# Kernel tuning notes

Measured on AMD Instinct MI355X. Metric: run time of the kernel, lower is better.

## Reference

```python
import jax, jax.numpy as jnp
import numpy as np

T, B, D = 256, 64, 512


def setup_inputs() -> dict:
    key = jax.random.key(0)
    ks = jax.random.split(key, 9)
    s = 1.0 / np.sqrt(D)  # torch Linear default init scale (uniform), use scaled normal
    return {
        "x": jax.random.normal(ks[0], (T, B, D), dtype=jnp.float32),
        "y": jax.random.normal(ks[1], (T, B, D), dtype=jnp.float32),
        "Wr": jax.random.normal(ks[2], (D, D), dtype=jnp.float32) * s,
        "Ur": jax.random.normal(ks[3], (D, D), dtype=jnp.float32) * s,
        "Wz": jax.random.normal(ks[4], (D, D), dtype=jnp.float32) * s,
        "Uz": jax.random.normal(ks[5], (D, D), dtype=jnp.float32) * s,
        "Wg": jax.random.normal(ks[6], (D, D), dtype=jnp.float32) * s,
        "Ug": jax.random.normal(ks[7], (D, D), dtype=jnp.float32) * s,
        "bg": jnp.full((D,), 2.0, dtype=jnp.float32),
    }


def reference(x, y, Wr, Ur, Wz, Uz, Wg, Ug, bg):
    # GTrXL gating unit. torch Linear(y) == y @ W.T
    r = jax.nn.sigmoid(jnp.einsum("tbd,ed->tbe", y, Wr) + jnp.einsum("tbd,ed->tbe", x, Ur))
    z = jax.nn.sigmoid(jnp.einsum("tbd,ed->tbe", y, Wz) + jnp.einsum("tbd,ed->tbe", x, Uz) - bg)
    h = jnp.tanh(jnp.einsum("tbd,ed->tbe", y, Wg) + jnp.einsum("tbd,ed->tbe", r * x, Ug))
    g = (1.0 - z) * x + z * h  # (T, B, D)
    return g
```

## Files before the change

kernel.cpp:

```cpp
#include <hip/hip_runtime.h>
#include <stdint.h>

typedef unsigned short u16;
typedef __attribute__((ext_vector_type(8))) __bf16 bf16x8;
typedef __attribute__((ext_vector_type(4))) float f32x4;

#define Dn 512
#define Mn 16384


__device__ __forceinline__ u16 f2bf(float f) {
  unsigned u = __float_as_uint(f);
  u += 0x7fffu + ((u >> 16) & 1u);
  return (u16)(u >> 16);
}

__device__ __forceinline__ float bf2f(u16 b) {
  return __uint_as_float(((unsigned)b) << 16);
}

__device__ __forceinline__ void async16(const u16* g, u16* l) {
  __builtin_amdgcn_global_load_lds(
      (const __attribute__((address_space(1))) unsigned int*)g,
      (__attribute__((address_space(3))) unsigned int*)l, 16, 0, 0);
}

__device__ __forceinline__ float sigmoidf_(float v) {
  return 1.f / (1.f + __expf(-v));
}

__global__ void cast_all(const float* __restrict__ y, const float* __restrict__ x,
                         const float* w0, const float* w1, const float* w2,
                         const float* w3, const float* w4, const float* w5,
                         u16* __restrict__ yb, u16* __restrict__ xb,
                         u16* __restrict__ bRZ, u16* __restrict__ bG) {
  int b = blockIdx.x;
  const int t = (int)threadIdx.x;
  if (b < 16384) {
    const float* src;
    u16* dst;
    if (b < 8192) { src = y; dst = yb; }
    else          { src = x; dst = xb; b -= 8192; }
    const int i4 = b * 256 + t;
    float4 v = ((const float4*)src)[i4];
    ushort4 o;
    o.x = f2bf(v.x); o.y = f2bf(v.y); o.z = f2bf(v.z); o.w = f2bf(v.w);
    ((ushort4*)dst)[i4] = o;
    return;
  }
  b -= 16384;
  const int wi = b >> 8;
  const int bb = b & 255;
  const float* src = wi == 0 ? w0 : wi == 1 ? w1 : wi == 2 ? w2
                   : wi == 3 ? w3 : wi == 4 ? w4 : w5;
  const int i4 = bb * 256 + t;
  const int e  = i4 >> 7;
  const int c4 = i4 & 127;
  float4 v = ((const float4*)src)[i4];
  ushort4 o;
  o.x = f2bf(v.x); o.y = f2bf(v.y); o.z = f2bf(v.z); o.w = f2bf(v.w);
  ushort4* base = (wi >= 4) ? (ushort4*)bG : (ushort4*)bRZ;
  const int row = e + ((wi == 2 || wi == 3) ? 512 : 0);
  const int off = row * 256 + c4 + ((wi & 1) ? 128 : 0);
  base[off] = o;
}

__global__ __launch_bounds__(512, 2) void gemm_rz2(
    const u16* __restrict__ yb, const u16* __restrict__ xb,
    const u16* __restrict__ bRZ, const float* __restrict__ bg,
    u16* __restrict__ rxb, u16* __restrict__ zb) {
  __shared__ u16 smem[65536];

  const int tid = threadIdx.x;
  const int lane = tid & 63;
  const int wave = tid >> 6;
  const int waveM = wave >> 2;
  const int waveN = wave & 3;
  const int mb = blockIdx.x & 63, nb = blockIdx.x >> 6;
  const int rowStart = mb * 256, colStart = nb * 256;
  const int lm = lane & 15, quad = lane >> 4;
  const int aoff = (quad ^ ((lm >> 1) & 3)) * 8;

  const int srow = tid >> 2;
  const int lc = ((tid & 3) ^ ((srow >> 1) & 3)) * 8;
  const int woff = wave * 1024;

  f32x4 acc[8][4] = {};

  auto STAGE = [&](int t) {
    const u16* abase = (t < 16) ? yb : xb;
    const int k0 = (t & 15) * 32;
    char* s = (char*)(smem + ((t & 3) << 14));
    async16(abase + (size_t)(rowStart + srow) * 512 + k0 + lc, (u16*)(s + woff));
    async16(abase + (size_t)(rowStart + 128 + srow) * 512 + k0 + lc, (u16*)(s + 8192 + woff));
    async16(bRZ + (size_t)(colStart + srow) * 1024 + t * 32 + lc, (u16*)(s + 16384 + woff));
    async16(bRZ + (size_t)(colStart + 128 + srow) * 1024 + t * 32 + lc, (u16*)(s + 24576 + woff));
  };

  STAGE(0); STAGE(1); STAGE(2); STAGE(3);
  __builtin_amdgcn_sched_barrier(0);

  for (int t = 0; t < 32; ++t) {
    if (t < 29)       asm volatile("s_waitcnt vmcnt(12)" ::: "memory");
    else if (t == 29) asm volatile("s_waitcnt vmcnt(8)" ::: "memory");
    else if (t == 30) asm volatile("s_waitcnt vmcnt(4)" ::: "memory");
    else              asm volatile("s_waitcnt vmcnt(0)" ::: "memory");
    __builtin_amdgcn_sched_barrier(0);
    __builtin_amdgcn_s_barrier();

    const u16* sA = smem + ((t & 3) << 14);
    const u16* sB = sA + 8192;
    bf16x8 aa[8], bw[4];
#pragma unroll
    for (int i = 0; i < 8; ++i)
      aa[i] = *(const bf16x8*)(sA + (waveM * 128 + i * 16 + lm) * 32 + aoff);
#pragma unroll
    for (int j = 0; j < 4; ++j)
      bw[j] = *(const bf16x8*)(sB + (waveN * 64 + j * 16 + lm) * 32 + aoff);
    asm volatile("s_waitcnt lgkmcnt(0)" ::: "memory");
    __builtin_amdgcn_sched_barrier(0);
    __builtin_amdgcn_s_barrier();

    if (t < 28) STAGE(t + 4);
    __builtin_amdgcn_sched_barrier(0);

    __builtin_amdgcn_s_setprio(1);
#pragma unroll
    for (int i = 0; i < 8; ++i)
#pragma unroll
      for (int j = 0; j < 4; ++j)
        acc[i][j] = __builtin_amdgcn_mfma_f32_16x16x32_bf16(aa[i], bw[j], acc[i][j], 0, 0, 0);
    __builtin_amdgcn_s_setprio(0);
  }

  if (colStart < 512) {
#pragma unroll
    for (int j = 0; j < 4; ++j) {
      const int e = colStart + waveN * 64 + j * 16 + lm;
#pragma unroll
      for (int i = 0; i < 8; ++i) {
        const int m0 = rowStart + waveM * 128 + i * 16 + quad * 4;
#pragma unroll
        for (int rg = 0; rg < 4; ++rg) {
          const size_t idx = (size_t)(m0 + rg) * 512 + e;
          const float r = sigmoidf_(acc[i][j][rg]);
          rxb[idx] = f2bf(r * bf2f(xb[idx]));
        }
      }
    }
  } else {
#pragma unroll
    for (int j = 0; j < 4; ++j) {
      const int e = colStart - 512 + waveN * 64 + j * 16 + lm;
      const float bgv = bg[e];
#pragma unroll
      for (int i = 0; i < 8; ++i) {
        const int m0 = rowStart + waveM * 128 + i * 16 + quad * 4;
#pragma unroll
        for (int rg = 0; rg < 4; ++rg) {
          const size_t idx = (size_t)(m0 + rg) * 512 + e;
          zb[idx] = f2bf(sigmoidf_(acc[i][j][rg] - bgv));
        }
      }
    }
  }
}

__global__ __launch_bounds__(256, 4) void gemm_gu1(
    const u16* __restrict__ yb, const u16* __restrict__ rxb,
    const u16* __restrict__ bG,
    const u16* __restrict__ zb, const u16* __restrict__ xb,
    float* __restrict__ out) {
  __shared__ u16 smem[16384];
  u16* sA = smem;
  u16* sB = smem + 8192;

  const int tid = threadIdx.x;
  const int lane = tid & 63;
  const int wave = tid >> 6;
  const int waveM = wave >> 1, waveN = wave & 1;
  const int mb = blockIdx.x & 127, nb = blockIdx.x >> 7;
  const int rowStart = mb * 128, colStart = nb * 128;
  const int wbyte = (tid & 192) * 16;
  const int lm = lane & 15, quad = lane >> 4;

  const int srow = tid >> 3;
  const int scol = (((tid & 7) ^ ((tid >> 3) & 7)) * 8);
  const int lswz = lm & 7;

  f32x4 acc[4][4] = {};

  for (int kq = 0; kq < 16; ++kq) {
    const int half = kq >> 3;
    const int k0 = (kq & 7) * 64;
    const u16* abase = half ? rxb : yb;
#pragma unroll
    for (int s = 0; s < 4; ++s) {
      async16(abase + (size_t)(rowStart + s * 32 + srow) * 512 + k0 + scol,
              (u16*)((char*)sA + s * 4096 + wbyte));
      async16(bG + (size_t)(colStart + s * 32 + srow) * 1024 + kq * 64 + scol,
              (u16*)((char*)sB + s * 4096 + wbyte));
    }
    __syncthreads();

#pragma unroll
    for (int kk = 0; kk < 2; ++kk) {
      bf16x8 aa[4], bw[4];
#pragma unroll
      for (int i = 0; i < 4; ++i)
        aa[i] = *(const bf16x8*)(sA + (waveM * 64 + i * 16 + lm) * 64 +
                                 ((kk * 4 + quad) ^ lswz) * 8);
#pragma unroll
      for (int j = 0; j < 4; ++j)
        bw[j] = *(const bf16x8*)(sB + (waveN * 64 + j * 16 + lm) * 64 +
                                 ((kk * 4 + quad) ^ lswz) * 8);
#pragma unroll
      for (int i = 0; i < 4; ++i)
#pragma unroll
        for (int j = 0; j < 4; ++j)
          acc[i][j] = __builtin_amdgcn_mfma_f32_16x16x32_bf16(aa[i], bw[j], acc[i][j], 0, 0, 0);
    }
    __syncthreads();
  }

#pragma unroll
  for (int j = 0; j < 4; ++j) {
    const int e = colStart + waveN * 64 + j * 16 + lm;
#pragma unroll
    for (int i = 0; i < 4; ++i) {
      const int m0 = rowStart + waveM * 64 + i * 16 + quad * 4;
#pragma unroll
      for (int rg = 0; rg < 4; ++rg) {
        const size_t idx = (size_t)(m0 + rg) * 512 + e;
        const float pre = acc[i][j][rg];
        const float ex = __expf(-2.f * pre);
        const float h = (1.f - ex) / (1.f + ex);
        const float z = bf2f(zb[idx]);
        const float xv = bf2f(xb[idx]);
        out[idx] = (1.f - z) * xv + z * h;
      }
    }
  }
}

extern "C" void kernel_launch(void* const* d_in, const int* in_sizes, int n_in,
                              void* d_out, int out_size, void* d_ws, size_t ws_size,
                              hipStream_t stream) {
  const float* x  = (const float*)d_in[0];
  const float* y  = (const float*)d_in[1];
  const float* Wr = (const float*)d_in[2];
  const float* Ur = (const float*)d_in[3];
  const float* Wz = (const float*)d_in[4];
  const float* Uz = (const float*)d_in[5];
  const float* Wg = (const float*)d_in[6];
  const float* Ug = (const float*)d_in[7];
  const float* bg = (const float*)d_in[8];
  float* out = (float*)d_out;

  char* ws = (char*)d_ws;
  u16* yb  = (u16*)(ws);
  u16* xb  = (u16*)(ws + 16777216);
  u16* rxb = (u16*)(ws + 2 * 16777216);
  u16* zb  = (u16*)(ws + 3 * 16777216);
  u16* bRZ = (u16*)(ws + 4 * 16777216);
  u16* bG  = (u16*)(ws + 4 * 16777216 + 2097152);

  cast_all<<<17920, 256, 0, stream>>>(y, x, Wr, Ur, Wz, Uz, Wg, Ug, yb, xb, bRZ, bG);
  gemm_rz2<<<256, 512, 0, stream>>>(yb, xb, bRZ, bg, rxb, zb);
  gemm_gu1<<<512, 256, 0, stream>>>(yb, rxb, bG, zb, xb, out);
}
```

Baseline: 212.5 us.

## Restructure r/z GEMM into K=64 double-buffered quadrant-interleaved pipeline

Rewrites the fused r/z GEMM main loop to use K=64 tiles over 16 iterations with two smem buffers, each split into four A/B half-tiles. Each iteration runs in four phases that read a quarter of the fragments, issue the next async global-to-LDS load and run a quarter of the MFMAs, so loads, LDS reads and math overlap more finely. The LDS swizzle changes to an 8-chunk XOR pattern. The cost is more barriers per iteration and a more complex vmcnt bookkeeping that could stall or mis-synchronise.

```diff
diff --git a/kernel.cpp b/kernel.cpp
--- a/kernel.cpp
+++ b/kernel.cpp
@@ -7,6 +7,7 @@
 
 #define Dn 512
 #define Mn 16384
+#define NT 16
 
 
 __device__ __forceinline__ u16 f2bf(float f) {
@@ -65,7 +66,7 @@
   base[off] = o;
 }
 
-__global__ __launch_bounds__(512, 2) void gemm_rz2(
+__global__ __launch_bounds__(512, 2) void gemm_rz3(
     const u16* __restrict__ yb, const u16* __restrict__ xb,
     const u16* __restrict__ bRZ, const float* __restrict__ bg,
     u16* __restrict__ rxb, u16* __restrict__ zb) {
@@ -74,72 +75,133 @@
   const int tid = threadIdx.x;
   const int lane = tid & 63;
   const int wave = tid >> 6;
-  const int waveM = wave >> 2;
-  const int waveN = wave & 3;
+  const int wm = wave >> 2;
+  const int wn = wave & 3;
   const int mb = blockIdx.x & 63, nb = blockIdx.x >> 6;
   const int rowStart = mb * 256, colStart = nb * 256;
   const int lm = lane & 15, quad = lane >> 4;
-  const int aoff = (quad ^ ((lm >> 1) & 3)) * 8;
-
-  const int srow = tid >> 2;
-  const int lc = ((tid & 3) ^ ((srow >> 1) & 3)) * 8;
-  const int woff = wave * 1024;
+  const int lswz = lm & 7;
+
+  const int sgrow = lane >> 3;
+  const int sgchunk = ((lane & 7) ^ sgrow) * 8;
+  const int ldsoff = wave * 512;
 
   f32x4 acc[8][4] = {};
-
-  auto STAGE = [&](int t) {
-    const u16* abase = (t < 16) ? yb : xb;
-    const int k0 = (t & 15) * 32;
-    char* s = (char*)(smem + ((t & 3) << 14));
-    async16(abase + (size_t)(rowStart + srow) * 512 + k0 + lc, (u16*)(s + woff));
-    async16(abase + (size_t)(rowStart + 128 + srow) * 512 + k0 + lc, (u16*)(s + 8192 + woff));
-    async16(bRZ + (size_t)(colStart + srow) * 1024 + t * 32 + lc, (u16*)(s + 16384 + woff));
-    async16(bRZ + (size_t)(colStart + 128 + srow) * 1024 + t * 32 + lc, (u16*)(s + 24576 + woff));
+  bf16x8 af[8];
+  bf16x8 bfr[8];
+
+  const u16* myA;
+  const u16* myB;
+
+  auto STG = [&](int v) {
+    const int tt = v >> 2, hid = v & 3;
+    if (tt >= NT) return;
+    u16* slot = smem + (((tt & 1) * 4 + ((hid + 2) & 3)) * 8192);
+    if (hid >= 2) {
+      const int a = hid - 2;
+      const u16* ab = (tt < 8) ? yb : xb;
+      const int k0 = (tt & 7) * 64;
+#pragma unroll
+      for (int s = 0; s < 2; ++s)
+        async16(ab + (size_t)(rowStart + a * 128 + s * 64 + wave * 8 + sgrow) * 512 + k0 + sgchunk,
+                slot + s * 4096 + ldsoff);
+    } else {
+      const int b = hid;
+#pragma unroll
+      for (int s = 0; s < 2; ++s)
+        async16(bRZ + (size_t)(colStart + b * 128 + s * 64 + wave * 8 + sgrow) * 1024 + tt * 64 + sgchunk,
+                slot + s * 4096 + ldsoff);
+    }
   };
 
-  STAGE(0); STAGE(1); STAGE(2); STAGE(3);
+  auto RD_A = [&](int ih) {
+#pragma unroll
+    for (int i2 = 0; i2 < 4; ++i2)
+#pragma unroll
+      for (int kk = 0; kk < 2; ++kk)
+        af[i2 * 2 + kk] = *(const bf16x8*)(myA + (ih * 64 + i2 * 16 + lm) * 64 +
+                                           (((kk * 4 + quad) ^ lswz) * 8));
+  };
+  auto RD_B = [&](int jh) {
+#pragma unroll
+    for (int j2 = 0; j2 < 2; ++j2)
+#pragma unroll
+      for (int kk = 0; kk < 2; ++kk)
+        bfr[(jh * 2 + j2) * 2 + kk] = *(const bf16x8*)(myB + ((jh * 2 + j2) * 16 + lm) * 64 +
+                                                       (((kk * 4 + quad) ^ lswz) * 8));
+  };
+  auto MMA = [&](int ih, int jh) {
+    __builtin_amdgcn_s_setprio(1);
+#pragma unroll
+    for (int i2 = 0; i2 < 4; ++i2)
+#pragma unroll
+      for (int j2 = 0; j2 < 2; ++j2)
+#pragma unroll
+        for (int kk = 0; kk < 2; ++kk)
+          acc[ih * 4 + i2][jh * 2 + j2] = __builtin_amdgcn_mfma_f32_16x16x32_bf16(
+              af[i2 * 2 + kk], bfr[(jh * 2 + j2) * 2 + kk], acc[ih * 4 + i2][jh * 2 + j2], 0, 0, 0);
+    __builtin_amdgcn_s_setprio(0);
+  };
+
+#pragma unroll
+  for (int v = 0; v < 6; ++v) STG(v);
   __builtin_amdgcn_sched_barrier(0);
-
-  for (int t = 0; t < 32; ++t) {
-    if (t < 29)       asm volatile("s_waitcnt vmcnt(12)" ::: "memory");
-    else if (t == 29) asm volatile("s_waitcnt vmcnt(8)" ::: "memory");
-    else if (t == 30) asm volatile("s_waitcnt vmcnt(4)" ::: "memory");
-    else              asm volatile("s_waitcnt vmcnt(0)" ::: "memory");
-    __builtin_amdgcn_sched_barrier(0);
-    __builtin_amdgcn_s_barrier();
-
-    const u16* sA = smem + ((t & 3) << 14);
-    const u16* sB = sA + 8192;
-    bf16x8 aa[8], bw[4];
-#pragma unroll
-    for (int i = 0; i < 8; ++i)
-      aa[i] = *(const bf16x8*)(sA + (waveM * 128 + i * 16 + lm) * 32 + aoff);
-#pragma unroll
-    for (int j = 0; j < 4; ++j)
-      bw[j] = *(const bf16x8*)(sB + (waveN * 64 + j * 16 + lm) * 32 + aoff);
+  asm volatile("s_waitcnt vmcnt(4)" ::: "memory");
+  __builtin_amdgcn_sched_barrier(0);
+  __builtin_amdgcn_s_barrier();
+
+#pragma unroll 2
+  for (int t = 0; t < NT; ++t) {
+    const u16* bufb = smem + (t & 1) * 32768;
+    myA = bufb + wm * 8192;
+    myB = bufb + (2 + (wn >> 1)) * 8192 + (wn & 1) * 4096;
+    const int P = t * 4;
+
+    RD_A(0); RD_B(0); STG(P + 6);
+    __builtin_amdgcn_sched_barrier(0);
+    __builtin_amdgcn_s_barrier();
     asm volatile("s_waitcnt lgkmcnt(0)" ::: "memory");
     __builtin_amdgcn_sched_barrier(0);
-    __builtin_amdgcn_s_barrier();
-
-    if (t < 28) STAGE(t + 4);
-    __builtin_amdgcn_sched_barrier(0);
-
-    __builtin_amdgcn_s_setprio(1);
-#pragma unroll
-    for (int i = 0; i < 8; ++i)
-#pragma unroll
-      for (int j = 0; j < 4; ++j)
-        acc[i][j] = __builtin_amdgcn_mfma_f32_16x16x32_bf16(aa[i], bw[j], acc[i][j], 0, 0, 0);
-    __builtin_amdgcn_s_setprio(0);
+    MMA(0, 0);
+    __builtin_amdgcn_sched_barrier(0);
+    __builtin_amdgcn_s_barrier();
+
+    RD_B(1); STG(P + 7);
+    __builtin_amdgcn_sched_barrier(0);
+    __builtin_amdgcn_s_barrier();
+    asm volatile("s_waitcnt lgkmcnt(0)" ::: "memory");
+    __builtin_amdgcn_sched_barrier(0);
+    MMA(0, 1);
+    __builtin_amdgcn_sched_barrier(0);
+    __builtin_amdgcn_s_barrier();
+
+    RD_A(1); STG(P + 8);
+    __builtin_amdgcn_sched_barrier(0);
+    __builtin_amdgcn_s_barrier();
+    asm volatile("s_waitcnt lgkmcnt(0)" ::: "memory");
+    __builtin_amdgcn_sched_barrier(0);
+    MMA(1, 1);
+    __builtin_amdgcn_sched_barrier(0);
+    __builtin_amdgcn_s_barrier();
+
+    STG(P + 9);
+    __builtin_amdgcn_sched_barrier(0);
+    __builtin_amdgcn_s_barrier();
+    MMA(1, 0);
+    __builtin_amdgcn_sched_barrier(0);
+    if (t < NT - 2)       { asm volatile("s_waitcnt vmcnt(4)" ::: "memory"); }
+    else if (t == NT - 2) { asm volatile("s_waitcnt vmcnt(0)" ::: "memory"); }
+    __builtin_amdgcn_sched_barrier(0);
+    __builtin_amdgcn_s_barrier();
   }
 
   if (colStart < 512) {
 #pragma unroll
     for (int j = 0; j < 4; ++j) {
-      const int e = colStart + waveN * 64 + j * 16 + lm;
+      const int e = colStart + wn * 64 + j * 16 + lm;
 #pragma unroll
       for (int i = 0; i < 8; ++i) {
-        const int m0 = rowStart + waveM * 128 + i * 16 + quad * 4;
+        const int m0 = rowStart + wm * 128 + i * 16 + quad * 4;
 #pragma unroll
         for (int rg = 0; rg < 4; ++rg) {
           const size_t idx = (size_t)(m0 + rg) * 512 + e;
@@ -151,11 +213,11 @@
   } else {
 #pragma unroll
     for (int j = 0; j < 4; ++j) {
-      const int e = colStart - 512 + waveN * 64 + j * 16 + lm;
+      const int e = colStart - 512 + wn * 64 + j * 16 + lm;
       const float bgv = bg[e];
 #pragma unroll
       for (int i = 0; i < 8; ++i) {
-        const int m0 = rowStart + waveM * 128 + i * 16 + quad * 4;
+        const int m0 = rowStart + wm * 128 + i * 16 + quad * 4;
 #pragma unroll
         for (int rg = 0; rg < 4; ++rg) {
           const size_t idx = (size_t)(m0 + rg) * 512 + e;
@@ -266,6 +328,6 @@
   u16* bG  = (u16*)(ws + 4 * 16777216 + 2097152);
 
   cast_all<<<17920, 256, 0, stream>>>(y, x, Wr, Ur, Wz, Uz, Wg, Ug, yb, xb, bRZ, bG);
-  gemm_rz2<<<256, 512, 0, stream>>>(yb, xb, bRZ, bg, rxb, zb);
+  gemm_rz3<<<256, 512, 0, stream>>>(yb, xb, bRZ, bg, rxb, zb);
   gemm_gu1<<<512, 256, 0, stream>>>(yb, rxb, bG, zb, xb, out);
 }
```

Result: no change. 210.0 us (-1.2%).
